# Kernel tuning notes

Hardware: AMD Instinct MI355X
Metric: run time of the kernel (lower is better)

The kernel has to match this reference:

```python
import jax, jax.numpy as jnp
import numpy as np

# NF4 codebook used by bitsandbytes (16 levels, normalized to [-1, 1])
NF4_CODE = jnp.array([
    -1.0, -0.6961928009986877, -0.5250730514526367, -0.39491748809814453,
    -0.28444138169288635, -0.18477343022823334, -0.09105003625154495, 0.0,
    0.07958029955625534, 0.16093020141124725, 0.24611230194568634,
    0.33791524171829224, 0.44070982933044434, 0.5626170039176941,
    0.7229568362236023, 1.0], dtype=jnp.float32)
BLOCKSIZE = 64  # bitsandbytes default 4-bit blocksize


def nf4_quant_dequant(w):
    """Simulate bnb NF4 quantize -> dequantize (per-block absmax scaling)."""
    shape = w.shape
    flat = w.reshape(-1, BLOCKSIZE)                     # [n_blocks, 64]
    absmax = jnp.max(jnp.abs(flat), axis=1, keepdims=True)
    normalized = flat / jnp.where(absmax == 0, 1.0, absmax)
    # nearest-codebook-value quantization via midpoint boundaries
    bounds = (NF4_CODE[:-1] + NF4_CODE[1:]) * 0.5       # [15]
    idx = jnp.searchsorted(bounds, normalized)          # [n_blocks, 64] in [0,15]
    return (NF4_CODE[idx] * absmax).reshape(shape)


def setup_inputs() -> dict:
    key = jax.random.key(0)
    k1, k2, k3, kx = jax.random.split(key, 4)
    D, H = 4096, 11008
    scale = 0.02  # typical transformer init scale
    w1 = jax.random.normal(k1, (H, D), jnp.float32) * scale
    w2 = jax.random.normal(k2, (H, D), jnp.float32) * scale
    w3 = jax.random.normal(k3, (D, H), jnp.float32) * scale
    x = jax.random.normal(kx, (2, 2048, D), jnp.float32)
    return {"x": x, "w1": w1, "w2": w2, "w3": w3}


def reference(x, w1, w2, w3):
    dq1 = nf4_quant_dequant(w1)   # [H, D]
    dq2 = nf4_quant_dequant(w2)   # [H, D]
    dq3 = nf4_quant_dequant(w3)   # [D, H]
    gate = jnp.einsum('bsd,hd->bsh', x, dq1)
    up = jnp.einsum('bsd,hd->bsh', x, dq2)
    h = jax.nn.silu(gate) * up
    return jnp.einsum('bsh,dh->bsd', h, dq3)
```

## Files before the change

kernel.cpp:

```cpp
#include <hip/hip_runtime.h>
#include <math.h>

typedef __attribute__((ext_vector_type(4))) float f32x4;
typedef __attribute__((ext_vector_type(8))) short bf16x8;

#define DI __device__ __forceinline__

DI unsigned short f32_to_bf16(float f) {
  unsigned int u = __float_as_uint(f);
  u += 0x7FFFu + ((u >> 16) & 1u);
  return (unsigned short)(u >> 16);
}

static constexpr float kCode[16] = {
    -1.0f, -0.6961928009986877f, -0.5250730514526367f, -0.39491748809814453f,
    -0.28444138169288635f, -0.18477343022823334f, -0.09105003625154495f, 0.0f,
    0.07958029955625534f, 0.16093020141124725f, 0.24611230194568634f,
    0.33791524171829224f, 0.44070982933044434f, 0.5626170039176941f,
    0.7229568362236023f, 1.0f};

__global__ void __launch_bounds__(256) k_dequant_nf4(
    const float* __restrict__ in, unsigned short* __restrict__ out, int n4) {
  int i = blockIdx.x * 256 + threadIdx.x;
  if (i >= n4) return;
  f32x4 v = reinterpret_cast<const f32x4*>(in)[i];
  float am = fmaxf(fmaxf(fabsf(v.x), fabsf(v.y)), fmaxf(fabsf(v.z), fabsf(v.w)));
  am = fmaxf(am, __shfl_xor(am, 1));
  am = fmaxf(am, __shfl_xor(am, 2));
  am = fmaxf(am, __shfl_xor(am, 4));
  am = fmaxf(am, __shfl_xor(am, 8));
  float scale = (am == 0.0f) ? 1.0f : am;
  unsigned short o[4];
#pragma unroll
  for (int j = 0; j < 4; ++j) {
    float nv = ((const float*)&v)[j] / scale;
    int idx = 0;
#pragma unroll
    for (int b = 0; b < 15; ++b)
      idx += (nv > 0.5f * (kCode[b] + kCode[b + 1])) ? 1 : 0;
    o[j] = f32_to_bf16(kCode[idx] * am);
  }
  reinterpret_cast<ushort4*>(out)[i] = make_ushort4(o[0], o[1], o[2], o[3]);
}

__global__ void __launch_bounds__(256) k_f32_to_bf16(
    const float* __restrict__ in, unsigned short* __restrict__ out, int n4) {
  int i = blockIdx.x * 256 + threadIdx.x;
  if (i >= n4) return;
  f32x4 v = reinterpret_cast<const f32x4*>(in)[i];
  reinterpret_cast<ushort4*>(out)[i] =
      make_ushort4(f32_to_bf16(v.x), f32_to_bf16(v.y), f32_to_bf16(v.z), f32_to_bf16(v.w));
}

DI void gload16(const void* g, void* l) {
  __builtin_amdgcn_global_load_lds(
      (const __attribute__((address_space(1))) void*)g,
      (__attribute__((address_space(3))) void*)l, 16, 0, 0);
}

DI void barrier_nodrain() {
  asm volatile("" ::: "memory");
  __builtin_amdgcn_s_barrier();
  asm volatile("" ::: "memory");
}

#define WAITV(N) asm volatile("s_waitcnt vmcnt(" #N ")" ::: "memory")

__global__ void __launch_bounds__(1024, 4) k_gemm_dual_swiglu(
    const unsigned short* __restrict__ X,
    const unsigned short* __restrict__ W1,
    const unsigned short* __restrict__ W2,
    unsigned short* __restrict__ H) {
  constexpr int K = 4096, N = 11008, NK = K / 32;
  __shared__ char ldsb[131072];

  const int tid = threadIdx.x;
  const int w = tid >> 6, l = tid & 63;

  const int bid = blockIdx.x;
  const int lt = (bid & 7) * 172 + (bid >> 3);
  const int mt = lt & 15, nt = lt >> 4;
  const int m0 = mt * 256, n0 = nt * 128;

  const int p = w & 7;
  const bool isGate = (w < 8);
  const int wr = p >> 1, wc = p & 1;

  const int lrow = l >> 2;
  const int kc8 = (((l & 3) ^ ((l >> 3) & 3)) << 3);
  const unsigned short* gsrc0;
  const unsigned short* gsrc1;
  int ldst0;
  if (w < 8) {
    gsrc0 = X + (size_t)(m0 + 32 * w + lrow) * K + kc8;
    gsrc1 = X + (size_t)(m0 + 32 * w + 16 + lrow) * K + kc8;
    ldst0 = 2 * w * 1024;
  } else if (w < 12) {
    gsrc0 = W1 + (size_t)(n0 + 32 * (w - 8) + lrow) * K + kc8;
    gsrc1 = W1 + (size_t)(n0 + 32 * (w - 8) + 16 + lrow) * K + kc8;
    ldst0 = 16384 + (w - 8) * 2048;
  } else {
    gsrc0 = W2 + (size_t)(n0 + 32 * (w - 12) + lrow) * K + kc8;
    gsrc1 = W2 + (size_t)(n0 + 32 * (w - 12) + 16 + lrow) * K + kc8;
    ldst0 = 24576 + (w - 12) * 2048;
  }

#define STG(t) { const int bo_ = (((t) & 3) << 15) + ldst0;          \
    gload16(gsrc0 + (size_t)(t) * 32, ldsb + bo_);                    \
    gload16(gsrc1 + (size_t)(t) * 32, ldsb + bo_ + 1024); }

  const int roff = (((l >> 4) ^ ((l >> 1) & 3)) << 4);
  const char* rdA = ldsb + (wr * 64 + (l & 15)) * 64 + roff;
  const char* rdB = ldsb + 16384 + (isGate ? 0 : 8192) +
                    (wc * 64 + (l & 15)) * 64 + roff;

  f32x4 acc[4][4] = {};

  STG(0); STG(1); STG(2);
  WAITV(4);
  barrier_nodrain();

  for (int t = 0; t < NK; ++t) {
    const int bo = (t & 3) << 15;
    if (t + 3 < NK) STG(t + 3);
    bf16x8 a[4], b[4];
#pragma unroll
    for (int m = 0; m < 4; ++m) a[m] = *(const bf16x8*)(rdA + bo + m * 1024);
#pragma unroll
    for (int n = 0; n < 4; ++n) b[n] = *(const bf16x8*)(rdB + bo + n * 1024);
    __builtin_amdgcn_s_setprio(1);
#pragma unroll
    for (int m = 0; m < 4; ++m)
#pragma unroll
      for (int n = 0; n < 4; ++n)
        acc[m][n] = __builtin_amdgcn_mfma_f32_16x16x32_bf16(a[m], b[n], acc[m][n], 0, 0, 0);
    __builtin_amdgcn_s_setprio(0);
    if (t + 3 < NK)      { WAITV(4); barrier_nodrain(); }
    else if (t + 2 < NK) { WAITV(2); barrier_nodrain(); }
    else if (t + 1 < NK) { WAITV(0); barrier_nodrain(); }
  }
#undef STG

  barrier_nodrain();
  char* xch = ldsb + p * 16384 + (isGate ? 0 : 8192);
#pragma unroll
  for (int m2 = 0; m2 < 2; ++m2)
#pragma unroll
    for (int n = 0; n < 4; ++n) {
      const int m = isGate ? (m2 + 2) : m2;
      *(f32x4*)(xch + ((m2 * 4 + n) * 64 + l) * 16) = acc[m][n];
    }
  barrier_nodrain();
  const char* oxch = ldsb + p * 16384 + (isGate ? 8192 : 0);
  const int er = (l >> 4) * 4, ec = l & 15;
#pragma unroll
  for (int m2 = 0; m2 < 2; ++m2)
#pragma unroll
    for (int n = 0; n < 4; ++n) {
      const int m = isGate ? m2 : (m2 + 2);
      f32x4 other = *(const f32x4*)(oxch + ((m2 * 4 + n) * 64 + l) * 16);
#pragma unroll
      for (int j = 0; j < 4; ++j) {
        const float g_ = isGate ? acc[m][n][j] : other[j];
        const float u_ = isGate ? other[j] : acc[m][n][j];
        const float s = g_ / (1.0f + expf(-g_));
        const int row = m0 + wr * 64 + m * 16 + er + j;
        const int col = n0 + wc * 64 + n * 16 + ec;
        H[(size_t)row * N + col] = f32_to_bf16(s * u_);
      }
    }
}

__global__ void __launch_bounds__(1024, 4) k_gemm_out(
    const unsigned short* __restrict__ Hm,
    const unsigned short* __restrict__ W3,
    float* __restrict__ Out) {
  constexpr int K = 11008, N = 4096, NK = K / 32;
  __shared__ char ldsb[131072];

  const int tid = threadIdx.x;
  const int w = tid >> 6, l = tid & 63;

  const int bid = blockIdx.x;
  const int lt = (bid & 7) * 32 + (bid >> 3);
  const int mt = lt & 15, nt = lt >> 4;
  const int m0 = mt * 256, n0 = nt * 256;

  const int wr = w >> 2, wc = w & 3;

  const int lrow = l >> 2;
  const int kc8 = (((l & 3) ^ ((l >> 3) & 3)) << 3);
  const unsigned short* gsrc0;
  const unsigned short* gsrc1;
  int ldst0;
  if (w < 8) {
    gsrc0 = Hm + (size_t)(m0 + 32 * w + lrow) * K + kc8;
    gsrc1 = Hm + (size_t)(m0 + 32 * w + 16 + lrow) * K + kc8;
    ldst0 = 2 * w * 1024;
  } else {
    gsrc0 = W3 + (size_t)(n0 + 32 * (w - 8) + lrow) * K + kc8;
    gsrc1 = W3 + (size_t)(n0 + 32 * (w - 8) + 16 + lrow) * K + kc8;
    ldst0 = 16384 + (w - 8) * 2048;
  }

#define STG(t) { const int bo_ = (((t) & 3) << 15) + ldst0;          \
    gload16(gsrc0 + (size_t)(t) * 32, ldsb + bo_);                    \
    gload16(gsrc1 + (size_t)(t) * 32, ldsb + bo_ + 1024); }

  const int roff = (((l >> 4) ^ ((l >> 1) & 3)) << 4);
  const char* rdA = ldsb + (wr * 64 + (l & 15)) * 64 + roff;
  const char* rdB = ldsb + 16384 + (wc * 64 + (l & 15)) * 64 + roff;

  f32x4 acc[4][4] = {};

  STG(0); STG(1); STG(2);
  WAITV(4);
  barrier_nodrain();

  for (int t = 0; t < NK; ++t) {
    const int bo = (t & 3) << 15;
    if (t + 3 < NK) STG(t + 3);
    bf16x8 a[4], b[4];
#pragma unroll
    for (int m = 0; m < 4; ++m) a[m] = *(const bf16x8*)(rdA + bo + m * 1024);
#pragma unroll
    for (int n = 0; n < 4; ++n) b[n] = *(const bf16x8*)(rdB + bo + n * 1024);
    __builtin_amdgcn_s_setprio(1);
#pragma unroll
    for (int m = 0; m < 4; ++m)
#pragma unroll
      for (int n = 0; n < 4; ++n)
        acc[m][n] = __builtin_amdgcn_mfma_f32_16x16x32_bf16(a[m], b[n], acc[m][n], 0, 0, 0);
    __builtin_amdgcn_s_setprio(0);
    if (t + 3 < NK)      { WAITV(4); barrier_nodrain(); }
    else if (t + 2 < NK) { WAITV(2); barrier_nodrain(); }
    else if (t + 1 < NK) { WAITV(0); barrier_nodrain(); }
  }
#undef STG

  const int er = (l >> 4) * 4, ec = l & 15;
#pragma unroll
  for (int m = 0; m < 4; ++m)
#pragma unroll
    for (int n = 0; n < 4; ++n) {
      const int row = m0 + wr * 64 + m * 16 + er;
      const int col = n0 + wc * 64 + n * 16 + ec;
      float* ptr = Out + (size_t)row * N + col;
#pragma unroll
      for (int j = 0; j < 4; ++j) ptr[(size_t)j * N] = acc[m][n][j];
    }
}

extern "C" void kernel_launch(void* const* d_in, const int* in_sizes, int n_in,
                              void* d_out, int out_size, void* d_ws, size_t ws_size,
                              hipStream_t stream) {
  const float* x  = (const float*)d_in[0];
  const float* w1 = (const float*)d_in[1];
  const float* w2 = (const float*)d_in[2];
  const float* w3 = (const float*)d_in[3];
  float* out = (float*)d_out;

  char* ws = (char*)d_ws;
  unsigned short* xb  = (unsigned short*)(ws);
  unsigned short* w1b = (unsigned short*)(ws + 33554432);
  unsigned short* w2b = (unsigned short*)(ws + 123731968);
  unsigned short* hb  = (unsigned short*)(ws + 213909504);
  unsigned short* w3b = w1b;

  const int NW = 11008 * 4096 / 4;
  k_f32_to_bf16<<<16384, 256, 0, stream>>>(x, xb, 4096 * 4096 / 4);
  k_dequant_nf4<<<NW / 256, 256, 0, stream>>>(w1, w1b, NW);
  k_dequant_nf4<<<NW / 256, 256, 0, stream>>>(w2, w2b, NW);

  k_gemm_dual_swiglu<<<1376, 1024, 0, stream>>>(xb, w1b, w2b, hb);

  k_dequant_nf4<<<NW / 256, 256, 0, stream>>>(w3, w3b, NW);

  k_gemm_out<<<256, 1024, 0, stream>>>(hb, w3b, out);
}
```

Baseline: 1.271 ms.

## Halve block size to 8 waves with 128x64 per-wave tiles and split-phase pipeline

Both GEMM kernels move from 16 waves (1024 threads) to 8 waves (512 threads). Each wave now computes twice as many output rows (8x4 MFMA tiles), which raises register reuse of the B fragments and halves the number of LDS reads of B per MFMA. The main loop is split into two half-phases that interleave the global-to-LDS staging with compute, using a prefetch depth of 2 instead of 3. The SwiGLU epilogue exchange is reworked so gate and up partner waves swap halves through LDS. The costs are higher accumulator register pressure (128 fp32 per lane), fewer waves to hide latency, and extra barriers per iteration.

```diff
diff --git a/kernel.cpp b/kernel.cpp
--- a/kernel.cpp
+++ b/kernel.cpp
@@ -66,7 +66,7 @@
 
 #define WAITV(N) asm volatile("s_waitcnt vmcnt(" #N ")" ::: "memory")
 
-__global__ void __launch_bounds__(1024, 4) k_gemm_dual_swiglu(
+__global__ void __launch_bounds__(512, 2) k_gemm_dual_swiglu(
     const unsigned short* __restrict__ X,
     const unsigned short* __restrict__ W1,
     const unsigned short* __restrict__ W2,
@@ -82,52 +82,41 @@
   const int mt = lt & 15, nt = lt >> 4;
   const int m0 = mt * 256, n0 = nt * 128;
 
-  const int p = w & 7;
-  const bool isGate = (w < 8);
-  const int wr = p >> 1, wc = p & 1;
+  const int wr = w >> 2, wc = w & 3;
 
   const int lrow = l >> 2;
   const int kc8 = (((l & 3) ^ ((l >> 3) & 3)) << 3);
-  const unsigned short* gsrc0;
-  const unsigned short* gsrc1;
-  int ldst0;
-  if (w < 8) {
-    gsrc0 = X + (size_t)(m0 + 32 * w + lrow) * K + kc8;
-    gsrc1 = X + (size_t)(m0 + 32 * w + 16 + lrow) * K + kc8;
-    ldst0 = 2 * w * 1024;
-  } else if (w < 12) {
-    gsrc0 = W1 + (size_t)(n0 + 32 * (w - 8) + lrow) * K + kc8;
-    gsrc1 = W1 + (size_t)(n0 + 32 * (w - 8) + 16 + lrow) * K + kc8;
-    ldst0 = 16384 + (w - 8) * 2048;
-  } else {
-    gsrc0 = W2 + (size_t)(n0 + 32 * (w - 12) + lrow) * K + kc8;
-    gsrc1 = W2 + (size_t)(n0 + 32 * (w - 12) + 16 + lrow) * K + kc8;
-    ldst0 = 24576 + (w - 12) * 2048;
-  }
-
-#define STG(t) { const int bo_ = (((t) & 3) << 15) + ldst0;          \
-    gload16(gsrc0 + (size_t)(t) * 32, ldsb + bo_);                    \
-    gload16(gsrc1 + (size_t)(t) * 32, ldsb + bo_ + 1024); }
+  const int arow = (w & 3) * 16 + (w >> 2) * 128;
+  const unsigned short* sA[2] = {
+      X + (size_t)(m0 + arow + lrow) * K + kc8,
+      X + (size_t)(m0 + 64 + arow + lrow) * K + kc8};
+  const unsigned short* sB[2] = {
+      W1 + (size_t)(n0 + 16 * w + lrow) * K + kc8,
+      W2 + (size_t)(n0 + 16 * w + lrow) * K + kc8};
+
+#define STG(t, h) { const int bo_ = ((t) & 3) * 32768 + (h) * 8192 + w * 1024; \
+    gload16(sA[h] + (size_t)(t) * 32, ldsb + bo_);                              \
+    gload16(sB[h] + (size_t)(t) * 32, ldsb + bo_ + 16384); }
 
   const int roff = (((l >> 4) ^ ((l >> 1) & 3)) << 4);
   const char* rdA = ldsb + (wr * 64 + (l & 15)) * 64 + roff;
-  const char* rdB = ldsb + 16384 + (isGate ? 0 : 8192) +
-                    (wc * 64 + (l & 15)) * 64 + roff;
-
-  f32x4 acc[4][4] = {};
-
-  STG(0); STG(1); STG(2);
+  const char* rdB = ldsb + 16384 + (wc * 64 + (l & 15)) * 64 + roff;
+
+  f32x4 acc[8][4] = {};
+  bf16x8 a[4], b[4];
+
+  STG(0, 0); STG(0, 1); STG(1, 0); STG(1, 1);
   WAITV(4);
   barrier_nodrain();
 
   for (int t = 0; t < NK; ++t) {
-    const int bo = (t & 3) << 15;
-    if (t + 3 < NK) STG(t + 3);
-    bf16x8 a[4], b[4];
+    const int bo = (t & 3) * 32768;
 #pragma unroll
     for (int m = 0; m < 4; ++m) a[m] = *(const bf16x8*)(rdA + bo + m * 1024);
 #pragma unroll
     for (int n = 0; n < 4; ++n) b[n] = *(const bf16x8*)(rdB + bo + n * 1024);
+    if (t + 2 < NK) STG(t + 2, 0);
+    barrier_nodrain();
     __builtin_amdgcn_s_setprio(1);
 #pragma unroll
     for (int m = 0; m < 4; ++m)
@@ -135,43 +124,62 @@
       for (int n = 0; n < 4; ++n)
         acc[m][n] = __builtin_amdgcn_mfma_f32_16x16x32_bf16(a[m], b[n], acc[m][n], 0, 0, 0);
     __builtin_amdgcn_s_setprio(0);
-    if (t + 3 < NK)      { WAITV(4); barrier_nodrain(); }
-    else if (t + 2 < NK) { WAITV(2); barrier_nodrain(); }
-    else if (t + 1 < NK) { WAITV(0); barrier_nodrain(); }
+    barrier_nodrain();
+#pragma unroll
+    for (int m = 0; m < 4; ++m) a[m] = *(const bf16x8*)(rdA + bo + 8192 + m * 1024);
+    if (t + 2 < NK) STG(t + 2, 1);
+    barrier_nodrain();
+    __builtin_amdgcn_s_setprio(1);
+#pragma unroll
+    for (int m = 0; m < 4; ++m)
+#pragma unroll
+      for (int n = 0; n < 4; ++n)
+        acc[m + 4][n] = __builtin_amdgcn_mfma_f32_16x16x32_bf16(a[m], b[n], acc[m + 4][n], 0, 0, 0);
+    __builtin_amdgcn_s_setprio(0);
+    if (t + 2 < NK)      { WAITV(4); }
+    else if (t + 1 < NK) { WAITV(0); }
+    barrier_nodrain();
   }
 #undef STG
 
+  const bool isGate = (wc < 2);
+  char* myreg = ldsb + w * 16384;
+  const char* pareg = ldsb + (w ^ 2) * 16384;
+#pragma unroll
+  for (int m2 = 0; m2 < 2; ++m2)
+#pragma unroll
+    for (int n = 0; n < 4; ++n) {
+      const int ms = isGate ? (m2 + 4) : m2;
+      *(f32x4*)(myreg + ((m2 * 4 + n) * 64 + l) * 16) = acc[ms][n];
+    }
+#pragma unroll
+  for (int m2 = 2; m2 < 4; ++m2)
+#pragma unroll
+    for (int n = 0; n < 4; ++n) {
+      const int ms = isGate ? (m2 + 4) : m2;
+      *(f32x4*)(myreg + ((m2 * 4 + n) * 64 + l) * 16) = acc[ms][n];
+    }
   barrier_nodrain();
-  char* xch = ldsb + p * 16384 + (isGate ? 0 : 8192);
-#pragma unroll
-  for (int m2 = 0; m2 < 2; ++m2)
-#pragma unroll
-    for (int n = 0; n < 4; ++n) {
-      const int m = isGate ? (m2 + 2) : m2;
-      *(f32x4*)(xch + ((m2 * 4 + n) * 64 + l) * 16) = acc[m][n];
-    }
-  barrier_nodrain();
-  const char* oxch = ldsb + p * 16384 + (isGate ? 8192 : 0);
   const int er = (l >> 4) * 4, ec = l & 15;
 #pragma unroll
-  for (int m2 = 0; m2 < 2; ++m2)
-#pragma unroll
-    for (int n = 0; n < 4; ++n) {
-      const int m = isGate ? m2 : (m2 + 2);
-      f32x4 other = *(const f32x4*)(oxch + ((m2 * 4 + n) * 64 + l) * 16);
+  for (int m2 = 0; m2 < 4; ++m2)
+#pragma unroll
+    for (int n = 0; n < 4; ++n) {
+      const int mk = isGate ? m2 : (m2 + 4);
+      f32x4 other = *(const f32x4*)(pareg + ((m2 * 4 + n) * 64 + l) * 16);
 #pragma unroll
       for (int j = 0; j < 4; ++j) {
-        const float g_ = isGate ? acc[m][n][j] : other[j];
-        const float u_ = isGate ? other[j] : acc[m][n][j];
+        const float g_ = isGate ? acc[mk][n][j] : other[j];
+        const float u_ = isGate ? other[j] : acc[mk][n][j];
         const float s = g_ / (1.0f + expf(-g_));
-        const int row = m0 + wr * 64 + m * 16 + er + j;
-        const int col = n0 + wc * 64 + n * 16 + ec;
+        const int row = m0 + wr * 128 + mk * 16 + er + j;
+        const int col = n0 + (wc & 1) * 64 + n * 16 + ec;
         H[(size_t)row * N + col] = f32_to_bf16(s * u_);
       }
     }
 }
 
-__global__ void __launch_bounds__(1024, 4) k_gemm_out(
+__global__ void __launch_bounds__(512, 2) k_gemm_out(
     const unsigned short* __restrict__ Hm,
     const unsigned short* __restrict__ W3,
     float* __restrict__ Out) {
@@ -190,41 +198,37 @@
 
   const int lrow = l >> 2;
   const int kc8 = (((l & 3) ^ ((l >> 3) & 3)) << 3);
-  const unsigned short* gsrc0;
-  const unsigned short* gsrc1;
-  int ldst0;
-  if (w < 8) {
-    gsrc0 = Hm + (size_t)(m0 + 32 * w + lrow) * K + kc8;
-    gsrc1 = Hm + (size_t)(m0 + 32 * w + 16 + lrow) * K + kc8;
-    ldst0 = 2 * w * 1024;
-  } else {
-    gsrc0 = W3 + (size_t)(n0 + 32 * (w - 8) + lrow) * K + kc8;
-    gsrc1 = W3 + (size_t)(n0 + 32 * (w - 8) + 16 + lrow) * K + kc8;
-    ldst0 = 16384 + (w - 8) * 2048;
-  }
-
-#define STG(t) { const int bo_ = (((t) & 3) << 15) + ldst0;          \
-    gload16(gsrc0 + (size_t)(t) * 32, ldsb + bo_);                    \
-    gload16(gsrc1 + (size_t)(t) * 32, ldsb + bo_ + 1024); }
+  const int arow = (w & 3) * 16 + (w >> 2) * 128;
+  const unsigned short* sA[2] = {
+      Hm + (size_t)(m0 + arow + lrow) * K + kc8,
+      Hm + (size_t)(m0 + 64 + arow + lrow) * K + kc8};
+  const unsigned short* sB[2] = {
+      W3 + (size_t)(n0 + 16 * w + lrow) * K + kc8,
+      W3 + (size_t)(n0 + 128 + 16 * w + lrow) * K + kc8};
+
+#define STG(t, h) { const int bo_ = ((t) & 3) * 32768 + (h) * 8192 + w * 1024; \
+    gload16(sA[h] + (size_t)(t) * 32, ldsb + bo_);                              \
+    gload16(sB[h] + (size_t)(t) * 32, ldsb + bo_ + 16384); }
 
   const int roff = (((l >> 4) ^ ((l >> 1) & 3)) << 4);
   const char* rdA = ldsb + (wr * 64 + (l & 15)) * 64 + roff;
   const char* rdB = ldsb + 16384 + (wc * 64 + (l & 15)) * 64 + roff;
 
-  f32x4 acc[4][4] = {};
-
-  STG(0); STG(1); STG(2);
+  f32x4 acc[8][4] = {};
+  bf16x8 a[4], b[4];
+
+  STG(0, 0); STG(0, 1); STG(1, 0); STG(1, 1);
   WAITV(4);
   barrier_nodrain();
 
   for (int t = 0; t < NK; ++t) {
-    const int bo = (t & 3) << 15;
-    if (t + 3 < NK) STG(t + 3);
-    bf16x8 a[4], b[4];
+    const int bo = (t & 3) * 32768;
 #pragma unroll
     for (int m = 0; m < 4; ++m) a[m] = *(const bf16x8*)(rdA + bo + m * 1024);
 #pragma unroll
     for (int n = 0; n < 4; ++n) b[n] = *(const bf16x8*)(rdB + bo + n * 1024);
+    if (t + 2 < NK) STG(t + 2, 0);
+    barrier_nodrain();
     __builtin_amdgcn_s_setprio(1);
 #pragma unroll
     for (int m = 0; m < 4; ++m)
@@ -232,18 +236,30 @@
       for (int n = 0; n < 4; ++n)
         acc[m][n] = __builtin_amdgcn_mfma_f32_16x16x32_bf16(a[m], b[n], acc[m][n], 0, 0, 0);
     __builtin_amdgcn_s_setprio(0);
-    if (t + 3 < NK)      { WAITV(4); barrier_nodrain(); }
-    else if (t + 2 < NK) { WAITV(2); barrier_nodrain(); }
-    else if (t + 1 < NK) { WAITV(0); barrier_nodrain(); }
+    barrier_nodrain();
+#pragma unroll
+    for (int m = 0; m < 4; ++m) a[m] = *(const bf16x8*)(rdA + bo + 8192 + m * 1024);
+    if (t + 2 < NK) STG(t + 2, 1);
+    barrier_nodrain();
+    __builtin_amdgcn_s_setprio(1);
+#pragma unroll
+    for (int m = 0; m < 4; ++m)
+#pragma unroll
+      for (int n = 0; n < 4; ++n)
+        acc[m + 4][n] = __builtin_amdgcn_mfma_f32_16x16x32_bf16(a[m], b[n], acc[m + 4][n], 0, 0, 0);
+    __builtin_amdgcn_s_setprio(0);
+    if (t + 2 < NK)      { WAITV(4); }
+    else if (t + 1 < NK) { WAITV(0); }
+    barrier_nodrain();
   }
 #undef STG
 
   const int er = (l >> 4) * 4, ec = l & 15;
 #pragma unroll
-  for (int m = 0; m < 4; ++m)
-#pragma unroll
-    for (int n = 0; n < 4; ++n) {
-      const int row = m0 + wr * 64 + m * 16 + er;
+  for (int m = 0; m < 8; ++m)
+#pragma unroll
+    for (int n = 0; n < 4; ++n) {
+      const int row = m0 + wr * 128 + m * 16 + er;
       const int col = n0 + wc * 64 + n * 16 + ec;
       float* ptr = Out + (size_t)row * N + col;
 #pragma unroll
@@ -272,9 +288,9 @@
   k_dequant_nf4<<<NW / 256, 256, 0, stream>>>(w1, w1b, NW);
   k_dequant_nf4<<<NW / 256, 256, 0, stream>>>(w2, w2b, NW);
 
-  k_gemm_dual_swiglu<<<1376, 1024, 0, stream>>>(xb, w1b, w2b, hb);
+  k_gemm_dual_swiglu<<<1376, 512, 0, stream>>>(xb, w1b, w2b, hb);
 
   k_dequant_nf4<<<NW / 256, 256, 0, stream>>>(w3, w3b, NW);
 
-  k_gemm_out<<<256, 1024, 0, stream>>>(hb, w3b, out);
-}
+  k_gemm_out<<<256, 512, 0, stream>>>(hb, w3b, out);
+}
```

Result: slower. 1.324 ms (+4.1%).

## Switch GEMM kernels from 16x16x32 to 32x32x16 bf16 MFMA tiles

Applied to the files above, without the earlier changes.

Both GEMM kernels now compute each wave's 64x64 tile with four 32x32x16 MFMA accumulators instead of sixteen 16x16x32 ones. The LDS read pattern, swizzle offsets and epilogue indexing are rewritten to match the 32x32 output layout. Global prefetch pointers are now advanced incrementally instead of recomputed per stage. The larger instruction halves the LDS fragment reads per k-step and may raise MFMA throughput, but it changes bank-conflict behaviour and gives a different epilogue store pattern.

```diff
diff --git a/kernel.cpp b/kernel.cpp
--- a/kernel.cpp
+++ b/kernel.cpp
@@ -2,6 +2,7 @@
 #include <math.h>
 
 typedef __attribute__((ext_vector_type(4))) float f32x4;
+typedef __attribute__((ext_vector_type(16))) float f32x16;
 typedef __attribute__((ext_vector_type(8))) short bf16x8;
 
 #define DI __device__ __forceinline__
@@ -53,7 +54,8 @@
 }
 
 DI void gload16(const void* g, void* l) {
-  __builtin_amdgcn_global_load_lds(
+  __builtin_amdgcn_global_lo\
+ad_lds(
       (const __attribute__((address_space(1))) void*)g,
       (__attribute__((address_space(3))) void*)l, 16, 0, 0);
 }
@@ -79,8 +81,8 @@
 
   const int bid = blockIdx.x;
   const int lt = (bid & 7) * 172 + (bid >> 3);
-  const int mt = lt & 15, nt = lt >> 4;
-  const int m0 = mt * 256, n0 = nt * 128;
+  const int mt = lt & 15, nt0 = lt >> 4;
+  const int m0 = mt * 256, n0 = nt0 * 128;
 
   const int p = w & 7;
   const bool isGate = (w < 8);
@@ -88,84 +90,107 @@
 
   const int lrow = l >> 2;
   const int kc8 = (((l & 3) ^ ((l >> 3) & 3)) << 3);
-  const unsigned short* gsrc0;
-  const unsigned short* gsrc1;
+  const unsigned short* g0;
+  const unsigned short* g1;
   int ldst0;
   if (w < 8) {
-    gsrc0 = X + (size_t)(m0 + 32 * w + lrow) * K + kc8;
-    gsrc1 = X + (size_t)(m0 + 32 * w + 16 + lrow) * K + kc8;
+    g0 = X + (size_t)(m0 + 32 * w + lrow) * K + kc8;
+    g1 = X + (size_t)(m0 + 32 * w + 16 + lrow) * K + kc8;
     ldst0 = 2 * w * 1024;
   } else if (w < 12) {
-    gsrc0 = W1 + (size_t)(n0 + 32 * (w - 8) + lrow) * K + kc8;
-    gsrc1 = W1 + (size_t)(n0 + 32 * (w - 8) + 16 + lrow) * K + kc8;
+    g0 = W1 + (size_t)(n0 + 32 * (w - 8) + lrow) * K + kc8;
+    g1 = W1 + (size_t)(n0 + 32 * (w - 8) + 16 + lrow) * K + kc8;
     ldst0 = 16384 + (w - 8) * 2048;
   } else {
-    gsrc0 = W2 + (size_t)(n0 + 32 * (w - 12) + lrow) * K + kc8;
-    gsrc1 = W2 + (size_t)(n0 + 32 * (w - 12) + 16 + lrow) * K + kc8;
+    g0 = W2 + (size_t)(n0 + 32 * (w - 12) + lrow) * K + kc8;
+    g1 = W2 + (size_t)(n0 + 32 * (w - 12) + 16 + lrow) * K + kc8;
     ldst0 = 24576 + (w - 12) * 2048;
   }
 
-#define STG(t) { const int bo_ = (((t) & 3) << 15) + ldst0;          \
-    gload16(gsrc0 + (size_t)(t) * 32, ldsb + bo_);                    \
-    gload16(gsrc1 + (size_t)(t) * 32, ldsb + bo_ + 1024); }
-
-  const int roff = (((l >> 4) ^ ((l >> 1) & 3)) << 4);
-  const char* rdA = ldsb + (wr * 64 + (l & 15)) * 64 + roff;
-  const char* rdB = ldsb + 16384 + (isGate ? 0 : 8192) +
-                    (wc * 64 + (l & 15)) * 64 + roff;
-
-  f32x4 acc[4][4] = {};
-
-  STG(0); STG(1); STG(2);
+  const int la31 = l & 31, kb = l >> 5;
+  const int sw = ((la31 >> 1) & 3);
+  const int o0 = (kb ^ sw) << 4;
+  const int o1 = o0 ^ 32;
+  const char* rdA = ldsb + (wr * 64 + la31) * 64;
+  const char* rdB = ldsb + 16384 + (isGate ? 0 : 8192) + (wc * 64 + la31) * 64;
+
+  f32x16 acc[2][2] = {};
+  bf16x8 a[2][2], b[2][2];
+
+  gload16(g0, ldsb + ldst0);                 gload16(g1, ldsb + ldst0 + 1024);
+  gload16(g0 + 32, ldsb + 32768 + ldst0);    gload16(g1 + 32, ldsb + 32768 + ldst0 + 1024);
+  gload16(g0 + 64, ldsb + 65536 + ldst0);    gload16(g1 + 64, ldsb + 65536 + ldst0 + 1024);
+  const unsigned short* p0 = g0 + 96;
+  const unsigned short* p1 = g1 + 96;
   WAITV(4);
   barrier_nodrain();
 
   for (int t = 0; t < NK; ++t) {
     const int bo = (t & 3) << 15;
-    if (t + 3 < NK) STG(t + 3);
-    bf16x8 a[4], b[4];
-#pragma unroll
-    for (int m = 0; m < 4; ++m) a[m] = *(const bf16x8*)(rdA + bo + m * 1024);
-#pragma unroll
-    for (int n = 0; n < 4; ++n) b[n] = *(const bf16x8*)(rdB + bo + n * 1024);
+    if (t + 3 < NK) {
+      const int bs = ((t + 3) & 3) << 15;
+      gload16(p0, ldsb + bs + ldst0);
+      gload16(p1, ldsb + bs + ldst0 + 1024);
+    }
+    p0 += 32; p1 += 32;
+#pragma unroll
+    for (int m = 0; m < 2; ++m) {
+      a[m][0] = *(const bf16x8*)(rdA + bo + m * 2048 + o0);
+      a[m][1] = *(const bf16x8*)(rdA + bo + m * 2048 + o1);
+    }
+#pragma unroll
+    for (int n = 0; n < 2; ++n) {
+      b[n][0] = *(const bf16x8*)(rdB + bo + n * 2048 + o0);
+      b[n][1] = *(const bf16x8*)(rdB + bo + n * 2048 + o1);
+    }
     __builtin_amdgcn_s_setprio(1);
 #pragma unroll
-    for (int m = 0; m < 4; ++m)
-#pragma unroll
-      for (int n = 0; n < 4; ++n)
-        acc[m][n] = __builtin_amdgcn_mfma_f32_16x16x32_bf16(a[m], b[n], acc[m][n], 0, 0, 0);
+    for (int kk = 0; kk < 2; ++kk)
+#pragma unroll
+      for (int m = 0; m < 2; ++m)
+#pragma unroll
+        for (int n = 0; n < 2; ++n)
+          acc[m][n] = __builtin_amdgcn_mfma_f32_32x32x16_bf16(a[m][kk], b[n][kk], acc[m][n], 0, 0, 0);
     __builtin_amdgcn_s_setprio(0);
     if (t + 3 < NK)      { WAITV(4); barrier_nodrain(); }
     else if (t + 2 < NK) { WAITV(2); barrier_nodrain(); }
     else if (t + 1 < NK) { WAITV(0); barrier_nodrain(); }
   }
-#undef STG
 
   barrier_nodrain();
-  char* xch = ldsb + p * 16384 + (isGate ? 0 : 8192);
-#pragma unroll
-  for (int m2 = 0; m2 < 2; ++m2)
-#pragma unroll
-    for (int n = 0; n < 4; ++n) {
-      const int m = isGate ? (m2 + 2) : m2;
-      *(f32x4*)(xch + ((m2 * 4 + n) * 64 + l) * 16) = acc[m][n];
+  char* myx = ldsb + w * 8192;
+  const char* px = ldsb + (w ^ 8) * 8192;
+#pragma unroll
+  for (int n = 0; n < 2; ++n)
+#pragma unroll
+    for (int q = 0; q < 4; ++q) {
+      f32x4 v;
+      if (isGate) {
+#pragma unroll
+        for (int jj = 0; jj < 4; ++jj) v[jj] = acc[1][n][4 * q + jj];
+      } else {
+#pragma unroll
+        for (int jj = 0; jj < 4; ++jj) v[jj] = acc[0][n][4 * q + jj];
+      }
+      *(f32x4*)(myx + ((n * 4 + q) * 64 + l) * 16) = v;
     }
   barrier_nodrain();
-  const char* oxch = ldsb + p * 16384 + (isGate ? 8192 : 0);
-  const int er = (l >> 4) * 4, ec = l & 15;
-#pragma unroll
-  for (int m2 = 0; m2 < 2; ++m2)
-#pragma unroll
-    for (int n = 0; n < 4; ++n) {
-      const int m = isGate ? m2 : (m2 + 2);
-      f32x4 other = *(const f32x4*)(oxch + ((m2 * 4 + n) * 64 + l) * 16);
-#pragma unroll
-      for (int j = 0; j < 4; ++j) {
-        const float g_ = isGate ? acc[m][n][j] : other[j];
-        const float u_ = isGate ? other[j] : acc[m][n][j];
+  const int smt = isGate ? 0 : 1;
+#pragma unroll
+  for (int n = 0; n < 2; ++n)
+#pragma unroll
+    for (int q = 0; q < 4; ++q) {
+      f32x4 other = *(const f32x4*)(px + ((n * 4 + q) * 64 + l) * 16);
+#pragma unroll
+      for (int jj = 0; jj < 4; ++jj) {
+        float mine;
+        if (isGate) mine = acc[0][n][4 * q + jj];
+        else        mine = acc[1][n][4 * q + jj];
+        const float g_ = isGate ? mine : other[jj];
+        const float u_ = isGate ? other[jj] : mine;
         const float s = g_ / (1.0f + expf(-g_));
-        const int row = m0 + wr * 64 + m * 16 + er + j;
-        const int col = n0 + wc * 64 + n * 16 + ec;
+        const int row = m0 + wr * 64 + smt * 32 + jj + 8 * q + 4 * kb;
+        const int col = n0 + wc * 64 + n * 32 + la31;
         H[(size_t)row * N + col] = f32_to_bf16(s * u_);
       }
     }
@@ -183,72 +208,88 @@
 
   const int bid = blockIdx.x;
   const int lt = (bid & 7) * 32 + (bid >> 3);
-  const int mt = lt & 15, nt = lt >> 4;
-  const int m0 = mt * 256, n0 = nt * 256;
+  const int mt = lt & 15, nt0 = lt >> 4;
+  const int m0 = mt * 256, n0 = nt0 * 256;
 
   const int wr = w >> 2, wc = w & 3;
 
   const int lrow = l >> 2;
   const int kc8 = (((l & 3) ^ ((l >> 3) & 3)) << 3);
-  const unsigned short* gsrc0;
-  const unsigned short* gsrc1;
+  const unsigned short* g0;
+  const unsigned short* g1;
   int ldst0;
   if (w < 8) {
-    gsrc0 = Hm + (size_t)(m0 + 32 * w + lrow) * K + kc8;
-    gsrc1 = Hm + (size_t)(m0 + 32 * w + 16 + lrow) * K + kc8;
+    g0 = Hm + (size_t)(m0 + 32 * w + lrow) * K + kc8;
+    g1 = Hm + (size_t)(m0 + 32 * w + 16 + lrow) * K + kc8;
     ldst0 = 2 * w * 1024;
   } else {
-    gsrc0 = W3 + (size_t)(n0 + 32 * (w - 8) + lrow) * K + kc8;
-    gsrc1 = W3 + (size_t)(n0 + 32 * (w - 8) + 16 + lrow) * K + kc8;
+    g0 = W3 + (size_t)(n0 + 32 * (w - 8) + lrow) * K + kc8;
+    g1 = W3 + (size_t)(n0 + 32 * (w - 8) + 16 + lrow) * K + kc8;
     ldst0 = 16384 + (w - 8) * 2048;
   }
 
-#define STG(t) { const int bo_ = (((t) & 3) << 15) + ldst0;          \
-    gload16(gsrc0 + (size_t)(t) * 32, ldsb + bo_);                    \
-    gload16(gsrc1 + (size_t)(t) * 32, ldsb + bo_ + 1024); }
-
-  const int roff = (((l >> 4) ^ ((l >> 1) & 3)) << 4);
-  const char* rdA = ldsb + (wr * 64 + (l & 15)) * 64 + roff;
-  const char* rdB = ldsb + 16384 + (wc * 64 + (l & 15)) * 64 + roff;
-
-  f32x4 acc[4][4] = {};
-
-  STG(0); STG(1); STG(2);
+  const int la31 = l & 31, kb = l >> 5;
+  const int sw = ((la31 >> 1) & 3);
+  const int o0 = (kb ^ sw) << 4;
+  const int o1 = o0 ^ 32;
+  const char* rdA = ldsb + (wr * 64 + la31) * 64;
+  const char* rdB = ldsb + 16384 + (wc * 64 + la31) * 64;
+
+  f32x16 acc[2][2] = {};
+  bf16x8 a[2][2], b[2][2];
+
+  gload16(g0, ldsb + ldst0);                 gload16(g1, ldsb + ldst0 + 1024);
+  gload16(g0 + 32, ldsb + 32768 + ldst0);    gload16(g1 + 32, ldsb + 32768 + ldst0 + 1024);
+  gload16(g0 + 64, ldsb + 65536 + ldst0);    gload16(g1 + 64, ldsb + 65536 + ldst0 + 1024);
+  const unsigned short* p0 = g0 + 96;
+  const unsigned short* p1 = g1 + 96;
   WAITV(4);
   barrier_nodrain();
 
   for (int t = 0; t < NK; ++t) {
     const int bo = (t & 3) << 15;
-    if (t + 3 < NK) STG(t + 3);
-    bf16x8 a[4], b[4];
-#pragma unroll
-    for (int m = 0; m < 4; ++m) a[m] = *(const bf16x8*)(rdA + bo + m * 1024);
-#pragma unroll
-    for (int n = 0; n < 4; ++n) b[n] = *(const bf16x8*)(rdB + bo + n * 1024);
+    if (t + 3 < NK) {
+      const int bs = ((t + 3) & 3) << 15;
+      gload16(p0, ldsb + bs + ldst0);
+      gload16(p1, ldsb + bs + ldst0 + 1024);
+    }
+    p0 += 32; p1 += 32;
+#pragma unroll
+    for (int m = 0; m < 2; ++m) {
+      a[m][0] = *(const bf16x8*)(rdA + bo + m * 2048 + o0);
+      a[m][1] = *(const bf16x8*)(rdA + bo + m * 2048 + o1);
+    }
+#pragma unroll
+    for (int n = 0; n < 2; ++n) {
+      b[n][0] = *(const bf16x8*)(rdB + bo + n * 2048 + o0);
+      b[n][1] = *(const bf16x8*)(rdB + bo + n * 2048 + o1);
+    }
     __builtin_amdgcn_s_setprio(1);
 #pragma unroll
-    for (int m = 0; m < 4; ++m)
-#pragma unroll
-      for (int n = 0; n < 4; ++n)
-        acc[m][n] = __builtin_amdgcn_mfma_f32_16x16x32_bf16(a[m], b[n], acc[m][n], 0, 0, 0);
+    for (int kk = 0; kk < 2; ++kk)
+#pragma unroll
+      for (int m = 0; m < 2; ++m)
+#pragma unroll
+        for (int n = 0; n < 2; ++n)
+          acc[m][n] = __builtin_amdgcn_mfma_f32_32x32x16_bf16(a[m][kk], b[n][kk], acc[m][n], 0, 0, 0);
     __builtin_amdgcn_s_setprio(0);
     if (t + 3 < NK)      { WAITV(4); barrier_nodrain(); }
     else if (t + 2 < NK) { WAITV(2); barrier_nodrain(); }
     else if (t + 1 < NK) { WAITV(0); barrier_nodrain(); }
   }
-#undef STG
-
-  const int er = (l >> 4) * 4, ec = l & 15;
-#pragma unroll
-  for (int m = 0; m < 4; ++m)
-#pragma unroll
-    for (int n = 0; n < 4; ++n) {
-      const int row = m0 + wr * 64 + m * 16 + er;
-      const int col = n0 + wc * 64 + n * 16 + ec;
-      float* ptr = Out + (size_t)row * N + col;
-#pragma unroll
-      for (int j = 0; j < 4; ++j) ptr[(size_t)j * N] = acc[m][n][j];
-    }
+
+#pragma unroll
+  for (int m = 0; m < 2; ++m)
+#pragma unroll
+    for (int n = 0; n < 2; ++n)
+#pragma unroll
+      for (int q = 0; q < 4; ++q)
+#pragma unroll
+        for (int jj = 0; jj < 4; ++jj) {
+          const int row = m0 + wr * 64 + m * 32 + jj + 8 * q + 4 * kb;
+          const int col = n0 + wc * 64 + n * 32 + la31;
+          Out[(size_t)row * N + col] = acc[m][n][4 * q + jj];
+        }
 }
 
 extern "C" void kernel_launch(void* const* d_in, const int* in_sizes, int n_in,
```

Measured after the change: 1.394 ms. 1.1x slower.
